# Kernel optimization log

Hardware: AMD Instinct MI355X
Metric: run time of the kernel (lower is better)

Reference implementation:

```python
import jax, jax.numpy as jnp
import numpy as np

N_NODES = 100000
N_EDGES = 3200000
IN_FEATS = 512
N_HIDDEN = 256
N_CLASSES = 16


def setup_inputs() -> dict:
    key = jax.random.key(0)
    k1, k2, k3, k4, k5, k6 = jax.random.split(key, 6)
    features = jax.random.normal(k1, (N_NODES, IN_FEATS), dtype=jnp.float32)
    edge_src = jax.random.randint(k2, (N_EDGES,), 0, N_NODES, dtype=jnp.int32)
    edge_dst = jax.random.randint(k3, (N_EDGES,), 0, N_NODES, dtype=jnp.int32)
    # Glorot-ish scaling for stability across 3 layers
    W1 = jax.random.normal(k4, (IN_FEATS, N_HIDDEN), dtype=jnp.float32) / np.sqrt(IN_FEATS)
    W2 = jax.random.normal(k5, (N_HIDDEN, N_HIDDEN), dtype=jnp.float32) / np.sqrt(N_HIDDEN)
    W3 = jax.random.normal(k6, (N_HIDDEN, N_CLASSES), dtype=jnp.float32) / np.sqrt(N_HIDDEN)
    return {"features": features, "edge_src": edge_src, "edge_dst": edge_dst,
            "W1": W1, "W2": W2, "W3": W3}


def graph_conv(feat, W, src, dst, n_nodes):
    # Dense projection (no bias), then copy_src + sum aggregation over edges.
    h = feat @ W                              # [N, out]
    msgs = h[src]                             # [E, out] gather from source nodes
    return jax.ops.segment_sum(msgs, dst, num_segments=n_nodes)  # [N, out]


def reference(features, edge_src, edge_dst, W1, W2, W3):
    h = graph_conv(features, W1, edge_src, edge_dst, N_NODES)
    h = graph_conv(h, W2, edge_src, edge_dst, N_NODES)
    h = graph_conv(h, W3, edge_src, edge_dst, N_NODES)
    return h
```

## Files before the change

kernel.cpp:

```cpp
#include <hip/hip_runtime.h>

#define NN 100000
#define NE 3200000
#define BS 512
#define NBUCK 196
#define EPB 12500

typedef short bf16x8 __attribute__((ext_vector_type(8)));
typedef float f32x4  __attribute__((ext_vector_type(4)));

__device__ inline unsigned rne_bf16(float x) {
    unsigned u = __float_as_uint(x);
    return (u + 0x7fffu + ((u >> 16) & 1u)) >> 16;
}
__device__ inline float bflo(unsigned u) { return __uint_as_float(u << 16); }
__device__ inline float bfhi(unsigned u) { return __uint_as_float(u & 0xffff0000u); }

__global__ __launch_bounds__(256) void l1_gemm_hist(const float* __restrict__ W2,
                                                    const float* __restrict__ W3,
                                                    float* __restrict__ M1,
                                                    const int* __restrict__ dst,
                                                    int* __restrict__ cntA) {
    __shared__ float As[16][260];
    __shared__ float Bs[256][16];
    __shared__ int hh[NBUCK];
    const int t = threadIdx.x;

    if (blockIdx.x < 16) {
        const int block_row = blockIdx.x * 16;
        for (int i = t; i < 1024; i += 256)
            ((float4*)&Bs[0][0])[i] = ((const float4*)W3)[i];
        for (int i = t; i < 1024; i += 256) {
            int idx = i << 2;
            int r = idx >> 8, c = idx & 255;
            int row = block_row + r;
            float4 v = ((const float4*)(W2 + (size_t)row * 256))[c >> 2];
            *(float4*)&As[r][c] = v;
        }
        __syncthreads();
        const int r = t >> 4, c = t & 15;
        float acc = 0.f;
#pragma unroll 8
        for (int k = 0; k < 256; ++k) acc += As[r][k] * Bs[k][c];
        M1[(size_t)(block_row + r) * 16 + c] = acc;
    } else {
        const int hb = blockIdx.x - 16;
        for (int i = t; i < NBUCK; i += 256) hh[i] = 0;
        __syncthreads();
        for (int e = hb * 256 + t; e < NE; e += 256 * 256)
            atomicAdd(&hh[dst[e] >> 9], 1);
        __syncthreads();
        for (int i = t; i < NBUCK; i += 256)
            if (hh[i]) atomicAdd(&cntA[i], hh[i]);
    }
}

__global__ __launch_bounds__(256) void gemm_n16t(const float* __restrict__ A,
                                                 const float* __restrict__ B,
                                                 unsigned short* __restrict__ Wt) {
    __shared__ float As[16][260];
    __shared__ float Bs[256][16];
    const int t = threadIdx.x;
    const int block_row = blockIdx.x * 16;

    for (int i = t; i < 1024; i += 256)
        ((float4*)&Bs[0][0])[i] = ((const float4*)B)[i];
    for (int i = t; i < 1024; i += 256) {
        int idx = i << 2;
        int r = idx >> 8, c = idx & 255;
        int row = block_row + r;
        float4 v = ((const float4*)(A + (size_t)row * 256))[c >> 2];
        *(float4*)&As[r][c] = v;
    }
    __syncthreads();
    const int r = t >> 4, c = t & 15;
    float acc = 0.f;
#pragma unroll 8
    for (int k = 0; k < 256; ++k) acc += As[r][k] * Bs[k][c];
    Wt[(size_t)c * 512 + block_row + r] = (unsigned short)rne_bf16(acc);
}

__global__ __launch_bounds__(512) void binA(const int* __restrict__ src,
                                            const int* __restrict__ dst,
                                            const int* __restrict__ cntA,
                                            int* __restrict__ cursorCnt,
                                            unsigned* __restrict__ packed) {
    __shared__ int sscan[256];
    __shared__ int baseL[NBUCK];
    __shared__ int hist[NBUCK];
    const int t = threadIdx.x;
    const int lo = blockIdx.x * EPB, hi = lo + EPB;

    int v = 0;
    if (t < 256) { v = (t < NBUCK) ? cntA[t] : 0; sscan[t] = v; }
    __syncthreads();
    for (int off = 1; off < 256; off <<= 1) {
        int u = 0;
        if (t < 256 && t >= off) u = sscan[t - off];
        __syncthreads();
        if (t < 256) sscan[t] += u;
        __syncthreads();
    }
    if (t < NBUCK) baseL[t] = sscan[t] - v;
    for (int i = t; i < NBUCK; i += 512) hist[i] = 0;
    __syncthreads();
    for (int i = lo + t; i < hi; i += 512)
        atomicAdd(&hist[dst[i] >> 9], 1);
    __syncthreads();
    for (int i = t; i < NBUCK; i += 512) {
        int c = hist[i];
        hist[i] = c ? baseL[i] + atomicAdd(&cursorCnt[i], c) : 0;
    }
    __syncthreads();
    for (int i = lo + t; i < hi; i += 512) {
        int d = dst[i];
        int pos = atomicAdd(&hist[d >> 9], 1);
        packed[pos] = ((unsigned)src[i] << 9) | (unsigned)(d & 511);
    }
}

__global__ __launch_bounds__(512) void gemm_xwc(const float* __restrict__ X,
                                                const unsigned short* __restrict__ WcT,
                                                unsigned short* __restrict__ Yb) {
    __shared__ unsigned short As[128][72];
    __shared__ unsigned short Ws[16][520];

    const int t = threadIdx.x;
    const int brow = blockIdx.x * 128;
    const int w = t >> 6, lane = t & 63;
    const int lrow = lane & 15, lk8 = (lane >> 4) * 8;

    for (int idx = t; idx < 1024; idx += 512) {
        int row = idx >> 6, ch = idx & 63;
        *(uint4*)&Ws[row][ch * 8] = ((const uint4*)(WcT + row * 512))[ch];
    }

    const int s_arow = t & 127, s_aq = t >> 7;
    const bool arow_ok = (brow + s_arow) < NN;
    const float* Ap0 = X + (size_t)(brow + s_arow) * 512 + s_aq * 16;

    f32x4 acc = {};

    for (int k0 = 0; k0 < 512; k0 += 64) {
        float4 f[4];
        if (arow_ok) {
            const float4* p = (const float4*)(Ap0 + k0);
#pragma unroll
            for (int i = 0; i < 4; ++i) f[i] = p[i];
        } else {
#pragma unroll
            for (int i = 0; i < 4; ++i) f[i] = make_float4(0.f, 0.f, 0.f, 0.f);
        }
        unsigned p8[8];
#pragma unroll
        for (int i = 0; i < 4; ++i) {
            p8[2 * i]     = rne_bf16(f[i].x) | (rne_bf16(f[i].y) << 16);
            p8[2 * i + 1] = rne_bf16(f[i].z) | (rne_bf16(f[i].w) << 16);
        }
        *(uint4*)&As[s_arow][s_aq * 16]     = make_uint4(p8[0], p8[1], p8[2], p8[3]);
        *(uint4*)&As[s_arow][s_aq * 16 + 8] = make_uint4(p8[4], p8[5], p8[6], p8[7]);
        __syncthreads();

#pragma unroll
        for (int ks = 0; ks < 2; ++ks) {
            bf16x8 af = *(const bf16x8*)&As[w * 16 + lrow][ks * 32 + lk8];
            bf16x8 bw = *(const bf16x8*)&Ws[lrow][k0 + ks * 32 + lk8];
            acc = __builtin_amdgcn_mfma_f32_16x16x32_bf16(af, bw, acc, 0, 0, 0);
        }
        __syncthreads();
    }

    const int col = lrow;
    const int rbase = brow + w * 16 + (lane >> 4) * 4;
#pragma unroll
    for (int r = 0; r < 4; ++r) {
        int row = rbase + r;
        if (row < NN)
            Yb[(size_t)row * 16 + col] = (unsigned short)rne_bf16(acc[r]);
    }
}

__global__ __launch_bounds__(512) void binB(const unsigned* __restrict__ packed,
                                            const int* __restrict__ cntA,
                                            int* __restrict__ offs,
                                            int* __restrict__ srcs) {
    __shared__ int sscan[256];
    __shared__ int h[512];
    __shared__ int run[512];
    const int b = blockIdx.x, t = threadIdx.x;

    int v = 0;
    if (t < 256) { v = (t < NBUCK) ? cntA[t] : 0; sscan[t] = v; }
    __syncthreads();
    for (int off = 1; off < 256; off <<= 1) {
        int u = 0;
        if (t < 256 && t >= off) u = sscan[t - off];
        __syncthreads();
        if (t < 256) sscan[t] += u;
        __syncthreads();
    }
    const int hi = sscan[b];
    const int lo = hi - cntA[b];

    h[t] = 0;
    __syncthreads();
    for (int i = lo + t; i < hi; i += 512)
        atomicAdd(&h[packed[i] & 511], 1);
    __syncthreads();
    int mine = h[t];
    for (int off = 1; off < 512; off <<= 1) {
        int u = (t >= off) ? h[t - off] : 0;
        __syncthreads();
        h[t] += u;
        __syncthreads();
    }
    int gbase = lo + (h[t] - mine);
    int node = b * BS + t;
    if (node < NN) offs[node] = gbase;
    run[t] = gbase;
    __syncthreads();
    for (int i = lo + t; i < hi; i += 512) {
        unsigned v2 = packed[i];
        int pos = atomicAdd(&run[v2 & 511], 1);
        srcs[pos] = (int)(v2 >> 9);
    }
    if (b == NBUCK - 1 && t == 0) offs[NN] = NE;
}

template<bool OUT_F32>
__global__ __launch_bounds__(256) void agg16(const unsigned short* __restrict__ h,
                                             const int* __restrict__ offs,
                                             const int* __restrict__ srcs,
                                             void* __restrict__ outp) {
    int tid = blockIdx.x * 256 + threadIdx.x;
    int node = tid >> 2, f4 = tid & 3;
    if (node >= NN) return;
    int beg = offs[node], end = offs[node + 1];
    float a0 = 0, a1 = 0, a2 = 0, a3 = 0;
    float b0 = 0, b1 = 0, b2 = 0, b3 = 0;
    float c0 = 0, c1 = 0, c2 = 0, c3 = 0;
    float d0 = 0, d1 = 0, d2 = 0, d3 = 0;
    int j = beg;
    for (; j + 4 <= end; j += 4) {
        int s0 = srcs[j], s1 = srcs[j + 1], s2 = srcs[j + 2], s3 = srcs[j + 3];
        uint2 u = *(const uint2*)(h + (size_t)s0 * 16 + f4 * 4);
        uint2 v = *(const uint2*)(h + (size_t)s1 * 16 + f4 * 4);
        uint2 w = *(const uint2*)(h + (size_t)s2 * 16 + f4 * 4);
        uint2 x = *(const uint2*)(h + (size_t)s3 * 16 + f4 * 4);
        a0 += bflo(u.x); a1 += bfhi(u.x); a2 += bflo(u.y); a3 += bfhi(u.y);
        b0 += bflo(v.x); b1 += bfhi(v.x); b2 += bflo(v.y); b3 += bfhi(v.y);
        c0 += bflo(w.x); c1 += bfhi(w.x); c2 += bflo(w.y); c3 += bfhi(w.y);
        d0 += bflo(x.x); d1 += bfhi(x.x); d2 += bflo(x.y); d3 += bfhi(x.y);
    }
    for (; j < end; ++j) {
        uint2 u = *(const uint2*)(h + (size_t)srcs[j] * 16 + f4 * 4);
        a0 += bflo(u.x); a1 += bfhi(u.x); a2 += bflo(u.y); a3 += bfhi(u.y);
    }
    float r0 = (a0 + b0) + (c0 + d0);
    float r1 = (a1 + b1) + (c1 + d1);
    float r2 = (a2 + b2) + (c2 + d2);
    float r3 = (a3 + b3) + (c3 + d3);
    if (OUT_F32) {
        ((float4*)outp)[(size_t)node * 4 + f4] = make_float4(r0, r1, r2, r3);
    } else {
        uint2 r;
        r.x = rne_bf16(r0) | (rne_bf16(r1) << 16);
        r.y = rne_bf16(r2) | (rne_bf16(r3) << 16);
        ((uint2*)outp)[(size_t)node * 4 + f4] = r;
    }
}

extern "C" void kernel_launch(void* const* d_in, const int* in_sizes, int n_in,
                              void* d_out, int out_size, void* d_ws, size_t ws_size,
                              hipStream_t stream) {
    const float* X   = (const float*)d_in[0];
    const int*   src = (const int*)d_in[1];
    const int*   dst = (const int*)d_in[2];
    const float* W1  = (const float*)d_in[3];
    const float* W2  = (const float*)d_in[4];
    const float* W3  = (const float*)d_in[5];
    float* out = (float*)d_out;

    char* ws = (char*)d_ws;
    unsigned short* Yb = (unsigned short*)ws;   ws += (size_t)NN * 16 * 2;
    unsigned short* Gb = (unsigned short*)ws;   ws += (size_t)NN * 16 * 2;
    float* M1 = (float*)ws;                     ws += 256 * 16 * 4;
    unsigned short* WcT = (unsigned short*)ws;  ws += 16 * 512 * 2;
    unsigned* packed = (unsigned*)ws;           ws += (size_t)NE * 4;
    int* srcs       = (int*)ws;                 ws += (size_t)NE * 4;
    int* offs       = (int*)ws;                 ws += ((size_t)NN + 4) * 4;
    int* cntA       = (int*)ws;                 ws += 256 * 4;
    int* cursorCnt  = (int*)ws;                 ws += 256 * 4;

    hipMemsetAsync(cntA, 0, 512 * 4, stream);

    l1_gemm_hist<<<16 + 256, 256, 0, stream>>>(W2, W3, M1, dst, cntA);

    gemm_n16t<<<32, 256, 0, stream>>>(W1, M1, WcT);

    binA<<<256, 512, 0, stream>>>(src, dst, cntA, cursorCnt, packed);

    gemm_xwc<<<(NN + 127) / 128, 512, 0, stream>>>(X, WcT, Yb);

    binB<<<NBUCK, 512, 0, stream>>>(packed, cntA, offs, srcs);

    const int agg_blocks = (NN * 4 + 255) / 256;
    agg16<false><<<agg_blocks, 256, 0, stream>>>(Yb, offs, srcs, Gb);
    agg16<false><<<agg_blocks, 256, 0, stream>>>(Gb, offs, srcs, Yb);
    agg16<true ><<<agg_blocks, 256, 0, stream>>>(Yb, offs, srcs, out);
}
```

Measured before the change: 235.3 us.

## Fuse weight-chain GEMMs into one prep block and unroll aggregation by eight

Merges the W2·W3 and W1·M1 weight-product kernels into the histogram kernel. A single block now computes both products serially, keeping the intermediate in shared memory, which removes one launch and the global M1 buffer. The aggregation kernel is unrolled from four to eight gathers per iteration to keep more independent loads in flight. The trade-off is that the 48 sub-GEMM steps, previously spread over 48 blocks, now run one after another in one block. That block could become the critical path of the prep kernel.

Result: slower. 410.0 us (+74.2%).

```diff
diff --git a/kernel.cpp b/kernel.cpp
--- a/kernel.cpp
+++ b/kernel.cpp
@@ -16,35 +16,55 @@
 __device__ inline float bflo(unsigned u) { return __uint_as_float(u << 16); }
 __device__ inline float bfhi(unsigned u) { return __uint_as_float(u & 0xffff0000u); }
 
-__global__ __launch_bounds__(256) void l1_gemm_hist(const float* __restrict__ W2,
-                                                    const float* __restrict__ W3,
-                                                    float* __restrict__ M1,
-                                                    const int* __restrict__ dst,
-                                                    int* __restrict__ cntA) {
+__global__ __launch_bounds__(256) void prep(const float* __restrict__ W1,
+                                            const float* __restrict__ W2,
+                                            const float* __restrict__ W3,
+                                            const int* __restrict__ dst,
+                                            int* __restrict__ cntA,
+                                            unsigned short* __restrict__ WcT) {
     __shared__ float As[16][260];
     __shared__ float Bs[256][16];
+    __shared__ float M1s[256][16];
     __shared__ int hh[NBUCK];
     const int t = threadIdx.x;
 
-    if (blockIdx.x < 16) {
-        const int block_row = blockIdx.x * 16;
+    if (blockIdx.x == 0) {
         for (int i = t; i < 1024; i += 256)
             ((float4*)&Bs[0][0])[i] = ((const float4*)W3)[i];
-        for (int i = t; i < 1024; i += 256) {
-            int idx = i << 2;
-            int r = idx >> 8, c = idx & 255;
-            int row = block_row + r;
-            float4 v = ((const float4*)(W2 + (size_t)row * 256))[c >> 2];
-            *(float4*)&As[r][c] = v;
-        }
         __syncthreads();
         const int r = t >> 4, c = t & 15;
-        float acc = 0.f;
+        for (int sb = 0; sb < 16; ++sb) {
+            const int row0 = sb * 16;
+            for (int i = t; i < 1024; i += 256) {
+                int idx = i << 2;
+                int rr = idx >> 8, cc = idx & 255;
+                float4 v = ((const float4*)(W2 + (size_t)(row0 + rr) * 256))[cc >> 2];
+                *(float4*)&As[rr][cc] = v;
+            }
+            __syncthreads();
+            float acc = 0.f;
 #pragma unroll 8
-        for (int k = 0; k < 256; ++k) acc += As[r][k] * Bs[k][c];
-        M1[(size_t)(block_row + r) * 16 + c] = acc;
+            for (int k = 0; k < 256; ++k) acc += As[r][k] * Bs[k][c];
+            M1s[row0 + r][c] = acc;
+            __syncthreads();
+        }
+        for (int sb = 0; sb < 32; ++sb) {
+            const int row0 = sb * 16;
+            for (int i = t; i < 1024; i += 256) {
+                int idx = i << 2;
+                int rr = idx >> 8, cc = idx & 255;
+                float4 v = ((const float4*)(W1 + (size_t)(row0 + rr) * 256))[cc >> 2];
+                *(float4*)&As[rr][cc] = v;
+            }
+            __syncthreads();
+            float acc = 0.f;
+#pragma unroll 8
+            for (int k = 0; k < 256; ++k) acc += As[r][k] * M1s[k][c];
+            WcT[(size_t)c * 512 + row0 + r] = (unsigned short)rne_bf16(acc);
+            __syncthreads();
+        }
     } else {
-        const int hb = blockIdx.x - 16;
+        const int hb = blockIdx.x - 1;
         for (int i = t; i < NBUCK; i += 256) hh[i] = 0;
         __syncthreads();
         for (int e = hb * 256 + t; e < NE; e += 256 * 256)
@@ -53,31 +73,6 @@
         for (int i = t; i < NBUCK; i += 256)
             if (hh[i]) atomicAdd(&cntA[i], hh[i]);
     }
-}
-
-__global__ __launch_bounds__(256) void gemm_n16t(const float* __restrict__ A,
-                                                 const float* __restrict__ B,
-                                                 unsigned short* __restrict__ Wt) {
-    __shared__ float As[16][260];
-    __shared__ float Bs[256][16];
-    const int t = threadIdx.x;
-    const int block_row = blockIdx.x * 16;
-
-    for (int i = t; i < 1024; i += 256)
-        ((float4*)&Bs[0][0])[i] = ((const float4*)B)[i];
-    for (int i = t; i < 1024; i += 256) {
-        int idx = i << 2;
-        int r = idx >> 8, c = idx & 255;
-        int row = block_row + r;
-        float4 v = ((const float4*)(A + (size_t)row * 256))[c >> 2];
-        *(float4*)&As[r][c] = v;
-    }
-    __syncthreads();
-    const int r = t >> 4, c = t & 15;
-    float acc = 0.f;
-#pragma unroll 8
-    for (int k = 0; k < 256; ++k) acc += As[r][k] * Bs[k][c];
-    Wt[(size_t)c * 512 + block_row + r] = (unsigned short)rne_bf16(acc);
 }
 
 __global__ __launch_bounds__(512) void binA(const int* __restrict__ src,
@@ -236,24 +231,34 @@
     int node = tid >> 2, f4 = tid & 3;
     if (node >= NN) return;
     int beg = offs[node], end = offs[node + 1];
+    const unsigned short* hp = h + f4 * 4;
     float a0 = 0, a1 = 0, a2 = 0, a3 = 0;
     float b0 = 0, b1 = 0, b2 = 0, b3 = 0;
     float c0 = 0, c1 = 0, c2 = 0, c3 = 0;
     float d0 = 0, d1 = 0, d2 = 0, d3 = 0;
     int j = beg;
-    for (; j + 4 <= end; j += 4) {
-        int s0 = srcs[j], s1 = srcs[j + 1], s2 = srcs[j + 2], s3 = srcs[j + 3];
-        uint2 u = *(const uint2*)(h + (size_t)s0 * 16 + f4 * 4);
-        uint2 v = *(const uint2*)(h + (size_t)s1 * 16 + f4 * 4);
-        uint2 w = *(const uint2*)(h + (size_t)s2 * 16 + f4 * 4);
-        uint2 x = *(const uint2*)(h + (size_t)s3 * 16 + f4 * 4);
-        a0 += bflo(u.x); a1 += bfhi(u.x); a2 += bflo(u.y); a3 += bfhi(u.y);
-        b0 += bflo(v.x); b1 += bfhi(v.x); b2 += bflo(v.y); b3 += bfhi(v.y);
-        c0 += bflo(w.x); c1 += bfhi(w.x); c2 += bflo(w.y); c3 += bfhi(w.y);
-        d0 += bflo(x.x); d1 += bfhi(x.x); d2 += bflo(x.y); d3 += bfhi(x.y);
+    for (; j + 8 <= end; j += 8) {
+        int s0 = srcs[j],     s1 = srcs[j + 1], s2 = srcs[j + 2], s3 = srcs[j + 3];
+        int s4 = srcs[j + 4], s5 = srcs[j + 5], s6 = srcs[j + 6], s7 = srcs[j + 7];
+        uint2 u0 = *(const uint2*)(hp + (size_t)s0 * 16);
+        uint2 u1 = *(const uint2*)(hp + (size_t)s1 * 16);
+        uint2 u2 = *(const uint2*)(hp + (size_t)s2 * 16);
+        uint2 u3 = *(const uint2*)(hp + (size_t)s3 * 16);
+        uint2 u4 = *(const uint2*)(hp + (size_t)s4 * 16);
+        uint2 u5 = *(const uint2*)(hp + (size_t)s5 * 16);
+        uint2 u6 = *(const uint2*)(hp + (size_t)s6 * 16);
+        uint2 u7 = *(const uint2*)(hp + (size_t)s7 * 16);
+        a0 += bflo(u0.x); a1 += bfhi(u0.x); a2 += bflo(u0.y); a3 += bfhi(u0.y);
+        b0 += bflo(u1.x); b1 += bfhi(u1.x); b2 += bflo(u1.y); b3 += bfhi(u1.y);
+        c0 += bflo(u2.x); c1 += bfhi(u2.x); c2 += bflo(u2.y); c3 += bfhi(u2.y);
+        d0 += bflo(u3.x); d1 += bfhi(u3.x); d2 += bflo(u3.y); d3 += bfhi(u3.y);
+        a0 += bflo(u4.x); a1 += bfhi(u4.x); a2 += bflo(u4.y); a3 += bfhi(u4.y);
+        b0 += bflo(u5.x); b1 += bfhi(u5.x); b2 += bflo(u5.y); b3 += bfhi(u5.y);
+        c0 += bflo(u6.x); c1 += bfhi(u6.x); c2 += bflo(u6.y); c3 += bfhi(u6.y);
+        d0 += bflo(u7.x); d1 += bfhi(u7.x); d2 += bflo(u7.y); d3 += bfhi(u7.y);
     }
     for (; j < end; ++j) {
-        uint2 u = *(const uint2*)(h + (size_t)srcs[j] * 16 + f4 * 4);
+        uint2 u = *(const uint2*)(hp + (size_t)srcs[j] * 16);
         a0 += bflo(u.x); a1 += bfhi(u.x); a2 += bflo(u.y); a3 += bfhi(u.y);
     }
     float r0 = (a0 + b0) + (c0 + d0);
@@ -284,7 +289,6 @@
     char* ws = (char*)d_ws;
     unsigned short* Yb = (unsigned short*)ws;   ws += (size_t)NN * 16 * 2;
     unsigned short* Gb = (unsigned short*)ws;   ws += (size_t)NN * 16 * 2;
-    float* M1 = (float*)ws;                     ws += 256 * 16 * 4;
     unsigned short* WcT = (unsigned short*)ws;  ws += 16 * 512 * 2;
     unsigned* packed = (unsigned*)ws;           ws += (size_t)NE * 4;
     int* srcs       = (int*)ws;                 ws += (size_t)NE * 4;
@@ -294,9 +298,7 @@
 
     hipMemsetAsync(cntA, 0, 512 * 4, stream);
 
-    l1_gemm_hist<<<16 + 256, 256, 0, stream>>>(W2, W3, M1, dst, cntA);
-
-    gemm_n16t<<<32, 256, 0, stream>>>(W1, M1, WcT);
+    prep<<<257, 256, 0, stream>>>(W1, W2, W3, dst, cntA, WcT);
 
     binA<<<256, 512, 0, stream>>>(src, dst, cntA, cursorCnt, packed);
 
```
